# Kernel optimization log

Hardware: AMD Instinct MI355X
Metric: run time of the kernel (lower is better)

Reference implementation:

```python
import jax, jax.numpy as jnp
import numpy as np

S, I, H = 4096, 2048, 2048


def setup_inputs() -> dict:
    key = jax.random.key(0)
    ks = jax.random.split(key, 7)
    k = 1.0 / np.sqrt(H)  # torch LSTMCell init range (values don't affect math shape)
    x = jax.random.normal(ks[0], (S, I), dtype=jnp.float32)
    W_ih = jax.random.uniform(ks[1], (4 * H, I), minval=-k, maxval=k, dtype=jnp.float32)
    W_hh = jax.random.uniform(ks[2], (4 * H, H), minval=-k, maxval=k, dtype=jnp.float32)
    b_ih = jax.random.uniform(ks[3], (4 * H,), minval=-k, maxval=k, dtype=jnp.float32)
    b_hh = jax.random.uniform(ks[4], (4 * H,), minval=-k, maxval=k, dtype=jnp.float32)
    xav = np.sqrt(2.0 / (1 + H))  # xavier_normal_ std for a (1, H) tensor
    h0 = jax.random.normal(ks[5], (1, H), dtype=jnp.float32) * xav
    c0 = jax.random.normal(ks[6], (1, H), dtype=jnp.float32) * xav
    return {"x": x, "W_ih": W_ih, "W_hh": W_hh, "b_ih": b_ih, "b_hh": b_hh, "h0": h0, "c0": c0}


def reference(x, W_ih, W_hh, b_ih, b_hh, h0, c0):
    # Precompute input contribution for all timesteps in one big GEMM: (S, 4H)
    x_gates = x @ W_ih.T + b_ih + b_hh
    W_hh_T = W_hh.T  # (H, 4H)

    def step(carry, xg_t):
        h, c = carry  # each (H,)
        gates = xg_t + h @ W_hh_T  # (4H,)
        i, f, g, o = jnp.split(gates, 4)
        i = jax.nn.sigmoid(i)
        f = jax.nn.sigmoid(f)
        g = jnp.tanh(g)
        o = jax.nn.sigmoid(o)
        c_new = f * c + i * g
        h_new = o * jnp.tanh(c_new)
        return (h_new, c_new), h_new

    _, hs = jax.lax.scan(step, (h0[0], c0[0]), x_gates)
    return hs[:, None, :]  # (S, 1, H) matching torch.stack of (1, H) states
```

## Files before the change

kernel.cpp:

```cpp
#include <hip/hip_runtime.h>
#include <hip/hip_bf16.h>

#define S_LEN 4096
#define IDIM  2048
#define HDIM  2048
#define G4    8192
#define NB    256
#define TPB   512
#define SENT  0x7FC00000u

typedef __attribute__((ext_vector_type(2))) float  f32x2;
typedef __attribute__((ext_vector_type(4))) float  f32x4;
typedef __attribute__((ext_vector_type(8))) short  bf16x8;

#define PKFMA(acc, w, h) \
  asm("v_pk_fma_f32 %0, %1, %2, %0" : "+v"(acc) : "v"(w), "v"(h))

__device__ __forceinline__ unsigned short f2bf(float f) {
  unsigned u = __float_as_uint(f);
  unsigned r = (u + 0x7FFFu + ((u >> 16) & 1u)) >> 16;
  return (unsigned short)r;
}
__device__ __forceinline__ float bf2f(unsigned short h) {
  return __uint_as_float(((unsigned)h) << 16);
}
__device__ __forceinline__ float sigmoid_fast(float x) {
  return __builtin_amdgcn_rcpf(1.f + __expf(-x));
}
__device__ __forceinline__ float tanh_fast(float x) {
  return 1.f - 2.f * __builtin_amdgcn_rcpf(__expf(2.f * x) + 1.f);
}

__global__ __launch_bounds__(256) void fill_sentinel(unsigned long long* p) {
  const unsigned long long v =
      ((unsigned long long)SENT << 32) | (unsigned long long)SENT;
  const int n = S_LEN * HDIM / 2;
  for (int i = blockIdx.x * 256 + threadIdx.x; i < n; i += gridDim.x * 256)
    p[i] = v;
}

#define BM 128
#define BKK 32
#define LDK 40

__global__ __launch_bounds__(256) void gemm_xg_mfma(
    const float* __restrict__ x, const float* __restrict__ Wih,
    const float* __restrict__ bih, const float* __restrict__ bhh,
    unsigned short* __restrict__ xg) {
  __shared__ unsigned short As[BM][LDK];
  __shared__ unsigned short Bs[BM][LDK];

  const int t = threadIdx.x;
  const int lane = t & 63, wid = t >> 6;
  const int wr = wid >> 1, wc = wid & 1;

  int bid = ((int)blockIdx.x & 7) * 256 + ((int)blockIdx.x >> 3);
  const int s0 = (bid >> 6) * BM;
  const int j0 = (bid & 63) * BM;

  f32x4 acc[4][4] = {};

  float bias[4];
#pragma unroll
  for (int n = 0; n < 4; ++n) {
    const int col = j0 + wc * 64 + n * 16 + (lane & 15);
    bias[n] = bih[col] + bhh[col];
  }

  for (int k0 = 0; k0 < IDIM; k0 += BKK) {
    float4 va[4], vb[4];
#pragma unroll
    for (int u = 0; u < 4; ++u) {
      const int f = t + 256 * u;
      const int row = f >> 3, kc = (f & 7) * 4;
      va[u] = *(const float4*)&x  [(size_t)(s0 + row) * IDIM + k0 + kc];
      vb[u] = *(const float4*)&Wih[(size_t)(j0 + row) * IDIM + k0 + kc];
    }
    __syncthreads();
#pragma unroll
    for (int u = 0; u < 4; ++u) {
      const int f = t + 256 * u;
      const int row = f >> 3, kc = (f & 7) * 4;
      ushort4 pa, pb;
      pa.x = f2bf(va[u].x); pa.y = f2bf(va[u].y);
      pa.z = f2bf(va[u].z); pa.w = f2bf(va[u].w);
      pb.x = f2bf(vb[u].x); pb.y = f2bf(vb[u].y);
      pb.z = f2bf(vb[u].z); pb.w = f2bf(vb[u].w);
      *(ushort4*)&As[row][kc] = pa;
      *(ushort4*)&Bs[row][kc] = pb;
    }
    __syncthreads();

    const int fr = lane & 15, koff = (lane >> 4) * 8;
    bf16x8 a[4], bfr[4];
#pragma unroll
    for (int m = 0; m < 4; ++m)
      a[m] = *(const bf16x8*)&As[wr * 64 + m * 16 + fr][koff];
#pragma unroll
    for (int n = 0; n < 4; ++n)
      bfr[n] = *(const bf16x8*)&Bs[wc * 64 + n * 16 + fr][koff];
#pragma unroll
    for (int m = 0; m < 4; ++m)
#pragma unroll
      for (int n = 0; n < 4; ++n)
        acc[m][n] = __builtin_amdgcn_mfma_f32_16x16x32_bf16(
            a[m], bfr[n], acc[m][n], 0, 0, 0);
  }

#pragma unroll
  for (int m = 0; m < 4; ++m) {
    const int row0 = s0 + wr * 64 + m * 16 + (lane >> 4) * 4;
#pragma unroll
    for (int n = 0; n < 4; ++n) {
      const int col = j0 + wc * 64 + n * 16 + (lane & 15);
#pragma unroll
      for (int r = 0; r < 4; ++r)
        xg[(size_t)(row0 + r) * G4 + col] = f2bf(acc[m][n][r] + bias[n]);
    }
  }
}

__global__ __launch_bounds__(TPB, 2) void lstm_scan(
    const unsigned short* __restrict__ xg, const float* __restrict__ Whh,
    const float* __restrict__ h0, const float* __restrict__ c0,
    float* __restrict__ out, unsigned* __restrict__ flags) {
  __shared__ __align__(16) float h_sh[HDIM];

  const int b = blockIdx.x, t = threadIdx.x;
  const int lane = t & 63, wid = t >> 6;
  const int j = b * 8 + wid;

  f32x2 w2[4][16];
#pragma unroll
  for (int g = 0; g < 4; ++g) {
    const float* wp = Whh + ((size_t)g * HDIM + j) * HDIM + lane * 4;
#pragma unroll
    for (int i = 0; i < 8; ++i) {
      const float4 v = *(const float4*)(wp + i * 256);
      w2[g][i * 2 + 0] = f32x2{v.x, v.y};
      w2[g][i * 2 + 1] = f32x2{v.z, v.w};
    }
  }
  float c_reg = (lane == 0) ? c0[j] : 0.f;

  for (int ts = 0; ts < S_LEN; ++ts) {
    float xgv = 0.f;
    if (lane < 4)
      xgv = bf2f(xg[(size_t)ts * G4 + (size_t)lane * HDIM + j]);

    if (ts == 0) {
      __syncthreads();
      h_sh[2*t]        = h0[2*t];
      h_sh[2*t + 1]    = h0[2*t + 1];
      h_sh[2*t + 1024] = h0[2*t + 1024];
      h_sh[2*t + 1025] = h0[2*t + 1025];
    } else {
      if (wid == 0) {
        const unsigned want = (unsigned)ts;
        unsigned f0 = 0, f1 = 0, f2 = 0, f3 = 0;
        for (;;) {
          if (f0 < want) f0 = __hip_atomic_load(&flags[lane],       __ATOMIC_RELAXED, __HIP_MEMORY_SCOPE_AGENT);
          if (f1 < want) f1 = __hip_atomic_load(&flags[lane +  64], __ATOMIC_RELAXED, __HIP_MEMORY_SCOPE_AGENT);
          if (f2 < want) f2 = __hip_atomic_load(&flags[lane + 128], __ATOMIC_RELAXED, __HIP_MEMORY_SCOPE_AGENT);
          if (f3 < want) f3 = __hip_atomic_load(&flags[lane + 192], __ATOMIC_RELAXED, __HIP_MEMORY_SCOPE_AGENT);
          if (f0 >= want && f1 >= want && f2 >= want && f3 >= want) break;
          __builtin_amdgcn_s_sleep(1);
        }
      }
      __syncthreads();
      const unsigned long long* src =
          (const unsigned long long*)(out + (size_t)(ts - 1) * HDIM);
      unsigned long long r0, r1;
      do {
        r0 = __hip_atomic_load(src + t, __ATOMIC_RELAXED,
                               __HIP_MEMORY_SCOPE_AGENT);
      } while (((unsigned)r0 == SENT) | ((unsigned)(r0 >> 32) == SENT));
      do {
        r1 = __hip_atomic_load(src + t + 512, __ATOMIC_RELAXED,
                               __HIP_MEMORY_SCOPE_AGENT);
      } while (((unsigned)r1 == SENT) | ((unsigned)(r1 >> 32) == SENT));
      h_sh[2*t]        = __uint_as_float((unsigned)r0);
      h_sh[2*t + 1]    = __uint_as_float((unsigned)(r0 >> 32));
      h_sh[2*t + 1024] = __uint_as_float((unsigned)r1);
      h_sh[2*t + 1025] = __uint_as_float((unsigned)(r1 >> 32));
    }
    __syncthreads();

    f32x2 A0 = {0.f, 0.f}, A1 = {0.f, 0.f}, A2 = {0.f, 0.f}, A3 = {0.f, 0.f};
    const f32x4* h4 = (const f32x4*)&h_sh[lane * 4];
#pragma unroll
    for (int i = 0; i < 8; ++i) {
      const f32x4 hv = h4[i * 64];
      const f32x2 hlo = {hv.x, hv.y}, hhi = {hv.z, hv.w};
      PKFMA(A0, w2[0][i*2+0], hlo); PKFMA(A0, w2[0][i*2+1], hhi);
      PKFMA(A1, w2[1][i*2+0], hlo); PKFMA(A1, w2[1][i*2+1], hhi);
      PKFMA(A2, w2[2][i*2+0], hlo); PKFMA(A2, w2[2][i*2+1], hhi);
      PKFMA(A3, w2[3][i*2+0], hlo); PKFMA(A3, w2[3][i*2+1], hhi);
    }
    float a0 = A0.x + A0.y, a1 = A1.x + A1.y;
    float a2 = A2.x + A2.y, a3 = A3.x + A3.y;
#pragma unroll
    for (int m = 1; m < 64; m <<= 1) {
      a0 += __shfl_xor(a0, m);
      a1 += __shfl_xor(a1, m);
      a2 += __shfl_xor(a2, m);
      a3 += __shfl_xor(a3, m);
    }
    float sv = (lane == 0) ? a0 : (lane == 1) ? a1 : (lane == 2) ? a2 : a3;
    sv += xgv;
    const float av = (lane == 2) ? tanh_fast(sv) : sigmoid_fast(sv);
    const float iv = __shfl(av, 0);
    const float fv = __shfl(av, 1);
    const float gv = __shfl(av, 2);
    const float ov = __shfl(av, 3);
    if (lane == 0) {
      c_reg = fmaf(fv, c_reg, iv * gv);
      const float hn = ov * tanh_fast(c_reg);
      __hip_atomic_store(&out[(size_t)ts * HDIM + j], hn,
                         __ATOMIC_RELAXED, __HIP_MEMORY_SCOPE_AGENT);
    }
    asm volatile("" ::: "memory");
    __builtin_amdgcn_s_barrier();
    asm volatile("" ::: "memory");
    if (t == 0)
      __hip_atomic_store(&flags[b], (unsigned)(ts + 1),
                         __ATOMIC_RELAXED, __HIP_MEMORY_SCOPE_AGENT);
  }
}

extern "C" void kernel_launch(void* const* d_in, const int* in_sizes, int n_in,
                              void* d_out, int out_size, void* d_ws, size_t ws_size,
                              hipStream_t stream) {
  const float* x   = (const float*)d_in[0];
  const float* Wih = (const float*)d_in[1];
  const float* Whh = (const float*)d_in[2];
  const float* bih = (const float*)d_in[3];
  const float* bhh = (const float*)d_in[4];
  const float* h0  = (const float*)d_in[5];
  const float* c0  = (const float*)d_in[6];
  float* out = (float*)d_out;

  unsigned* flags = (unsigned*)d_ws;
  unsigned short* xg = (unsigned short*)((char*)d_ws + 32768);

  hipMemsetAsync(flags, 0, NB * sizeof(unsigned), stream);

  fill_sentinel<<<dim3(2048), 256, 0, stream>>>((unsigned long long*)out);
  gemm_xg_mfma<<<dim3(2048), 256, 0, stream>>>(x, Wih, bih, bhh, xg);

  void* args[] = {(void*)&xg, (void*)&Whh, (void*)&h0,
                  (void*)&c0, (void*)&out, (void*)&flags};
  hipLaunchCooperativeKernel((void*)lstm_scan, dim3(NB), dim3(TPB),
                             args, 0, stream);
}
```

Before: 12.23 ms.

## Store recurrent weights as packed bf16 in registers and restage h layout

```diff
diff --git a/kernel.cpp b/kernel.cpp
--- a/kernel.cpp
+++ b/kernel.cpp
@@ -23,6 +23,15 @@
 }
 __device__ __forceinline__ float bf2f(unsigned short h) {
   return __uint_as_float(((unsigned)h) << 16);
+}
+__device__ __forceinline__ f32x2 bfpair(unsigned u) {
+  f32x2 r;
+  r.x = __uint_as_float(u << 16);
+  r.y = __uint_as_float(u & 0xFFFF0000u);
+  return r;
+}
+__device__ __forceinline__ f32x2 mk2(float a, float b) {
+  f32x2 r; r.x = a; r.y = b; return r;
 }
 __device__ __forceinline__ float sigmoid_fast(float x) {
   return __builtin_amdgcn_rcpf(1.f + __expf(-x));
@@ -120,83 +129,86 @@
   }
 }
 
+
+__device__ __forceinline__ void stage_pair(float* hA, float* hB, int k,
+                                           float v0, float v1) {
+  const int c = k >> 9, r = (k >> 3) & 63, e = k & 7;
+  float* dst = ((e & 4) ? hB : hA) + c * 256 + r * 4 + (e & 3);
+  dst[0] = v0;
+  dst[1] = v1;
+}
+
+#define DGC(Acc, g, c, HA, HB) do {                       \
+  const uint4 wv = w_reg[(g) * 4 + (c)];                  \
+  PKFMA(Acc, bfpair(wv.x), mk2(HA.x, HA.y));              \
+  PKFMA(Acc, bfpair(wv.y), mk2(HA.z, HA.w));              \
+  PKFMA(Acc, bfpair(wv.z), mk2(HB.x, HB.y));              \
+  PKFMA(Acc, bfpair(wv.w), mk2(HB.z, HB.w));              \
+} while (0)
+
 __global__ __launch_bounds__(TPB, 2) void lstm_scan(
     const unsigned short* __restrict__ xg, const float* __restrict__ Whh,
     const float* __restrict__ h0, const float* __restrict__ c0,
     float* __restrict__ out, unsigned* __restrict__ flags) {
-  __shared__ __align__(16) float h_sh[HDIM];
+  __shared__ __align__(16) float hA[1024];
+  __shared__ __align__(16) float hB[1024];
 
   const int b = blockIdx.x, t = threadIdx.x;
   const int lane = t & 63, wid = t >> 6;
   const int j = b * 8 + wid;
 
-  f32x2 w2[4][16];
+  uint4 w_reg[16];
 #pragma unroll
   for (int g = 0; g < 4; ++g) {
-    const float* wp = Whh + ((size_t)g * HDIM + j) * HDIM + lane * 4;
-#pragma unroll
-    for (int i = 0; i < 8; ++i) {
-      const float4 v = *(const float4*)(wp + i * 256);
-      w2[g][i * 2 + 0] = f32x2{v.x, v.y};
-      w2[g][i * 2 + 1] = f32x2{v.z, v.w};
-    }
-  }
+    const float* wp = Whh + ((size_t)g * HDIM + j) * HDIM;
+#pragma unroll
+    for (int c = 0; c < 4; ++c) {
+      const float4 q0 = *(const float4*)(wp + c * 512 + lane * 8);
+      const float4 q1 = *(const float4*)(wp + c * 512 + lane * 8 + 4);
+      uint4 pk;
+      pk.x = (unsigned)f2bf(q0.x) | ((unsigned)f2bf(q0.y) << 16);
+      pk.y = (unsigned)f2bf(q0.z) | ((unsigned)f2bf(q0.w) << 16);
+      pk.z = (unsigned)f2bf(q1.x) | ((unsigned)f2bf(q1.y) << 16);
+      pk.w = (unsigned)f2bf(q1.z) | ((unsigned)f2bf(q1.w) << 16);
+      asm volatile("" : "+v"(pk.x), "+v"(pk.y), "+v"(pk.z), "+v"(pk.w));
+      w_reg[g * 4 + c] = pk;
+    }
+  }
+
   float c_reg = (lane == 0) ? c0[j] : 0.f;
+
+  {
+    const float2 p0 = *(const float2*)&h0[2 * t];
+    const float2 p1 = *(const float2*)&h0[2 * t + 1024];
+    stage_pair(hA, hB, 2 * t, p0.x, p0.y);
+    stage_pair(hA, hB, 2 * t + 1024, p1.x, p1.y);
+  }
+  __syncthreads();
 
   for (int ts = 0; ts < S_LEN; ++ts) {
     float xgv = 0.f;
     if (lane < 4)
       xgv = bf2f(xg[(size_t)ts * G4 + (size_t)lane * HDIM + j]);
 
-    if (ts == 0) {
-      __syncthreads();
-      h_sh[2*t]        = h0[2*t];
-      h_sh[2*t + 1]    = h0[2*t + 1];
-      h_sh[2*t + 1024] = h0[2*t + 1024];
-      h_sh[2*t + 1025] = h0[2*t + 1025];
-    } else {
-      if (wid == 0) {
-        const unsigned want = (unsigned)ts;
-        unsigned f0 = 0, f1 = 0, f2 = 0, f3 = 0;
-        for (;;) {
-          if (f0 < want) f0 = __hip_atomic_load(&flags[lane],       __ATOMIC_RELAXED, __HIP_MEMORY_SCOPE_AGENT);
-          if (f1 < want) f1 = __hip_atomic_load(&flags[lane +  64], __ATOMIC_RELAXED, __HIP_MEMORY_SCOPE_AGENT);
-          if (f2 < want) f2 = __hip_atomic_load(&flags[lane + 128], __ATOMIC_RELAXED, __HIP_MEMORY_SCOPE_AGENT);
-          if (f3 < want) f3 = __hip_atomic_load(&flags[lane + 192], __ATOMIC_RELAXED, __HIP_MEMORY_SCOPE_AGENT);
-          if (f0 >= want && f1 >= want && f2 >= want && f3 >= want) break;
-          __builtin_amdgcn_s_sleep(1);
-        }
-      }
-      __syncthreads();
-      const unsigned long long* src =
-          (const unsigned long long*)(out + (size_t)(ts - 1) * HDIM);
-      unsigned long long r0, r1;
-      do {
-        r0 = __hip_atomic_load(src + t, __ATOMIC_RELAXED,
-                               __HIP_MEMORY_SCOPE_AGENT);
-      } while (((unsigned)r0 == SENT) | ((unsigned)(r0 >> 32) == SENT));
-      do {
-        r1 = __hip_atomic_load(src + t + 512, __ATOMIC_RELAXED,
-                               __HIP_MEMORY_SCOPE_AGENT);
-      } while (((unsigned)r1 == SENT) | ((unsigned)(r1 >> 32) == SENT));
-      h_sh[2*t]        = __uint_as_float((unsigned)r0);
-      h_sh[2*t + 1]    = __uint_as_float((unsigned)(r0 >> 32));
-      h_sh[2*t + 1024] = __uint_as_float((unsigned)r1);
-      h_sh[2*t + 1025] = __uint_as_float((unsigned)(r1 >> 32));
-    }
-    __syncthreads();
+    const f32x4 ha0 = *(const f32x4*)&hA[0 * 256 + lane * 4];
+    const f32x4 ha1 = *(const f32x4*)&hA[1 * 256 + lane * 4];
+    const f32x4 ha2 = *(const f32x4*)&hA[2 * 256 + lane * 4];
+    const f32x4 ha3 = *(const f32x4*)&hA[3 * 256 + lane * 4];
+    const f32x4 hb0 = *(const f32x4*)&hB[0 * 256 + lane * 4];
+    const f32x4 hb1 = *(const f32x4*)&hB[1 * 256 + lane * 4];
+    const f32x4 hb2 = *(const f32x4*)&hB[2 * 256 + lane * 4];
+    const f32x4 hb3 = *(const f32x4*)&hB[3 * 256 + lane * 4];
 
     f32x2 A0 = {0.f, 0.f}, A1 = {0.f, 0.f}, A2 = {0.f, 0.f}, A3 = {0.f, 0.f};
-    const f32x4* h4 = (const f32x4*)&h_sh[lane * 4];
-#pragma unroll
-    for (int i = 0; i < 8; ++i) {
-      const f32x4 hv = h4[i * 64];
-      const f32x2 hlo = {hv.x, hv.y}, hhi = {hv.z, hv.w};
-      PKFMA(A0, w2[0][i*2+0], hlo); PKFMA(A0, w2[0][i*2+1], hhi);
-      PKFMA(A1, w2[1][i*2+0], hlo); PKFMA(A1, w2[1][i*2+1], hhi);
-      PKFMA(A2, w2[2][i*2+0], hlo); PKFMA(A2, w2[2][i*2+1], hhi);
-      PKFMA(A3, w2[3][i*2+0], hlo); PKFMA(A3, w2[3][i*2+1], hhi);
-    }
+    DGC(A0, 0, 0, ha0, hb0); DGC(A0, 0, 1, ha1, hb1);
+    DGC(A0, 0, 2, ha2, hb2); DGC(A0, 0, 3, ha3, hb3);
+    DGC(A1, 1, 0, ha0, hb0); DGC(A1, 1, 1, ha1, hb1);
+    DGC(A1, 1, 2, ha2, hb2); DGC(A1, 1, 3, ha3, hb3);
+    DGC(A2, 2, 0, ha0, hb0); DGC(A2, 2, 1, ha1, hb1);
+    DGC(A2, 2, 2, ha2, hb2); DGC(A2, 2, 3, ha3, hb3);
+    DGC(A3, 3, 0, ha0, hb0); DGC(A3, 3, 1, ha1, hb1);
+    DGC(A3, 3, 2, ha2, hb2); DGC(A3, 3, 3, ha3, hb3);
+
     float a0 = A0.x + A0.y, a1 = A1.x + A1.y;
     float a2 = A2.x + A2.y, a3 = A3.x + A3.y;
 #pragma unroll
@@ -219,12 +231,42 @@
       __hip_atomic_store(&out[(size_t)ts * HDIM + j], hn,
                          __ATOMIC_RELAXED, __HIP_MEMORY_SCOPE_AGENT);
     }
-    asm volatile("" ::: "memory");
     __builtin_amdgcn_s_barrier();
-    asm volatile("" ::: "memory");
     if (t == 0)
       __hip_atomic_store(&flags[b], (unsigned)(ts + 1),
                          __ATOMIC_RELAXED, __HIP_MEMORY_SCOPE_AGENT);
+
+    if (ts + 1 == S_LEN) break;
+
+    if (wid == 0) {
+      const unsigned want = (unsigned)(ts + 1);
+      unsigned f0 = 0, f1 = 0, f2 = 0, f3 = 0;
+      for (;;) {
+        if (f0 < want) f0 = __hip_atomic_load(&flags[lane],       __ATOMIC_RELAXED, __HIP_MEMORY_SCOPE_AGENT);
+        if (f1 < want) f1 = __hip_atomic_load(&flags[lane +  64], __ATOMIC_RELAXED, __HIP_MEMORY_SCOPE_AGENT);
+        if (f2 < want) f2 = __hip_atomic_load(&flags[lane + 128], __ATOMIC_RELAXED, __HIP_MEMORY_SCOPE_AGENT);
+        if (f3 < want) f3 = __hip_atomic_load(&flags[lane + 192], __ATOMIC_RELAXED, __HIP_MEMORY_SCOPE_AGENT);
+        if (f0 >= want && f1 >= want && f2 >= want && f3 >= want) break;
+        __builtin_amdgcn_s_sleep(1);
+      }
+    }
+    __syncthreads();
+    const unsigned long long* src =
+        (const unsigned long long*)(out + (size_t)ts * HDIM);
+    unsigned long long r0, r1;
+    do {
+      r0 = __hip_atomic_load(src + t, __ATOMIC_RELAXED,
+                             __HIP_MEMORY_SCOPE_AGENT);
+    } while (((unsigned)r0 == SENT) | ((unsigned)(r0 >> 32) == SENT));
+    do {
+      r1 = __hip_atomic_load(src + t + 512, __ATOMIC_RELAXED,
+                             __HIP_MEMORY_SCOPE_AGENT);
+    } while (((unsigned)r1 == SENT) | ((unsigned)(r1 >> 32) == SENT));
+    stage_pair(hA, hB, 2 * t,
+               __uint_as_float((unsigned)r0), __uint_as_float((unsigned)(r0 >> 32)));
+    stage_pair(hA, hB, 2 * t + 1024,
+               __uint_as_float((unsigned)r1), __uint_as_float((unsigned)(r1 >> 32)));
+    __syncthreads();
   }
 }
 
```

New measurement: 18.89 ms. +54.5%, slower.

## Stage bf16 W_hh in LDS and prefetch weights during the inter-block wait

Applied to the files above, without the earlier changes.

```diff
diff --git a/kernel.cpp b/kernel.cpp
--- a/kernel.cpp
+++ b/kernel.cpp
@@ -23,6 +23,15 @@
 }
 __device__ __forceinline__ float bf2f(unsigned short h) {
   return __uint_as_float(((unsigned)h) << 16);
+}
+__device__ __forceinline__ f32x2 bfpair(unsigned u) {
+  f32x2 r;
+  r.x = __uint_as_float(u << 16);
+  r.y = __uint_as_float(u & 0xFFFF0000u);
+  return r;
+}
+__device__ __forceinline__ f32x2 mk2(float a, float b) {
+  f32x2 r; r.x = a; r.y = b; return r;
 }
 __device__ __forceinline__ float sigmoid_fast(float x) {
   return __builtin_amdgcn_rcpf(1.f + __expf(-x));
@@ -120,83 +129,92 @@
   }
 }
 
-__global__ __launch_bounds__(TPB, 2) void lstm_scan(
+
+#define LDW(g, i) \
+  (*(const uint4*)&Wlds[(wid * 4 + (g)) * 2048 + (i) * 512 + lane * 8])
+#define PIN4(v) \
+  asm volatile("" : "+v"(v.x), "+v"(v.y), "+v"(v.z), "+v"(v.w))
+#define WPREF do { \
+  w00 = LDW(0,0); w01 = LDW(0,1); w02 = LDW(0,2); w03 = LDW(0,3); \
+  w10 = LDW(1,0); w11 = LDW(1,1); w12 = LDW(1,2); w13 = LDW(1,3); \
+  w20 = LDW(2,0); w21 = LDW(2,1); w22 = LDW(2,2); w23 = LDW(2,3); \
+  w30 = LDW(3,0); w31 = LDW(3,1); w32 = LDW(3,2); w33 = LDW(3,3); \
+  PIN4(w00); PIN4(w01); PIN4(w02); PIN4(w03); \
+  PIN4(w10); PIN4(w11); PIN4(w12); PIN4(w13); \
+  PIN4(w20); PIN4(w21); PIN4(w22); PIN4(w23); \
+  PIN4(w30); PIN4(w31); PIN4(w32); PIN4(w33); \
+} while (0)
+
+#define DGC(Acc, W, HA, HB) do { \
+  PKFMA(Acc, bfpair(W.x), mk2(HA.x, HA.y)); \
+  PKFMA(Acc, bfpair(W.y), mk2(HA.z, HA.w)); \
+  PKFMA(Acc, bfpair(W.z), mk2(HB.x, HB.y)); \
+  PKFMA(Acc, bfpair(W.w), mk2(HB.z, HB.w)); \
+} while (0)
+
+__global__ __launch_bounds__(TPB, 1) void lstm_scan(
     const unsigned short* __restrict__ xg, const float* __restrict__ Whh,
     const float* __restrict__ h0, const float* __restrict__ c0,
     float* __restrict__ out, unsigned* __restrict__ flags) {
+  extern __shared__ unsigned short Wlds[];
   __shared__ __align__(16) float h_sh[HDIM];
 
   const int b = blockIdx.x, t = threadIdx.x;
   const int lane = t & 63, wid = t >> 6;
   const int j = b * 8 + wid;
 
-  f32x2 w2[4][16];
 #pragma unroll
   for (int g = 0; g < 4; ++g) {
-    const float* wp = Whh + ((size_t)g * HDIM + j) * HDIM + lane * 4;
-#pragma unroll
-    for (int i = 0; i < 8; ++i) {
-      const float4 v = *(const float4*)(wp + i * 256);
-      w2[g][i * 2 + 0] = f32x2{v.x, v.y};
-      w2[g][i * 2 + 1] = f32x2{v.z, v.w};
-    }
-  }
+    const float* wp = Whh + ((size_t)g * HDIM + j) * HDIM;
+#pragma unroll
+    for (int i = 0; i < 4; ++i) {
+      const float4 q0 = *(const float4*)(wp + i * 512 + lane * 8);
+      const float4 q1 = *(const float4*)(wp + i * 512 + lane * 8 + 4);
+      uint4 pk;
+      pk.x = (unsigned)f2bf(q0.x) | ((unsigned)f2bf(q0.y) << 16);
+      pk.y = (unsigned)f2bf(q0.z) | ((unsigned)f2bf(q0.w) << 16);
+      pk.z = (unsigned)f2bf(q1.x) | ((unsigned)f2bf(q1.y) << 16);
+      pk.w = (unsigned)f2bf(q1.z) | ((unsigned)f2bf(q1.w) << 16);
+      *(uint4*)&Wlds[(wid * 4 + g) * 2048 + i * 512 + lane * 8] = pk;
+    }
+  }
+
+  h_sh[t]        = h0[t];
+  h_sh[t + 512]  = h0[t + 512];
+  h_sh[t + 1024] = h0[t + 1024];
+  h_sh[t + 1536] = h0[t + 1536];
+  __syncthreads();
+
   float c_reg = (lane == 0) ? c0[j] : 0.f;
+
+  uint4 w00, w01, w02, w03, w10, w11, w12, w13,
+        w20, w21, w22, w23, w30, w31, w32, w33;
+  WPREF;
 
   for (int ts = 0; ts < S_LEN; ++ts) {
     float xgv = 0.f;
     if (lane < 4)
       xgv = bf2f(xg[(size_t)ts * G4 + (size_t)lane * HDIM + j]);
 
-    if (ts == 0) {
-      __syncthreads();
-      h_sh[2*t]        = h0[2*t];
-      h_sh[2*t + 1]    = h0[2*t + 1];
-      h_sh[2*t + 1024] = h0[2*t + 1024];
-      h_sh[2*t + 1025] = h0[2*t + 1025];
-    } else {
-      if (wid == 0) {
-        const unsigned want = (unsigned)ts;
-        unsigned f0 = 0, f1 = 0, f2 = 0, f3 = 0;
-        for (;;) {
-          if (f0 < want) f0 = __hip_atomic_load(&flags[lane],       __ATOMIC_RELAXED, __HIP_MEMORY_SCOPE_AGENT);
-          if (f1 < want) f1 = __hip_atomic_load(&flags[lane +  64], __ATOMIC_RELAXED, __HIP_MEMORY_SCOPE_AGENT);
-          if (f2 < want) f2 = __hip_atomic_load(&flags[lane + 128], __ATOMIC_RELAXED, __HIP_MEMORY_SCOPE_AGENT);
-          if (f3 < want) f3 = __hip_atomic_load(&flags[lane + 192], __ATOMIC_RELAXED, __HIP_MEMORY_SCOPE_AGENT);
-          if (f0 >= want && f1 >= want && f2 >= want && f3 >= want) break;
-          __builtin_amdgcn_s_sleep(1);
-        }
-      }
-      __syncthreads();
-      const unsigned long long* src =
-          (const unsigned long long*)(out + (size_t)(ts - 1) * HDIM);
-      unsigned long long r0, r1;
-      do {
-        r0 = __hip_atomic_load(src + t, __ATOMIC_RELAXED,
-                               __HIP_MEMORY_SCOPE_AGENT);
-      } while (((unsigned)r0 == SENT) | ((unsigned)(r0 >> 32) == SENT));
-      do {
-        r1 = __hip_atomic_load(src + t + 512, __ATOMIC_RELAXED,
-                               __HIP_MEMORY_SCOPE_AGENT);
-      } while (((unsigned)r1 == SENT) | ((unsigned)(r1 >> 32) == SENT));
-      h_sh[2*t]        = __uint_as_float((unsigned)r0);
-      h_sh[2*t + 1]    = __uint_as_float((unsigned)(r0 >> 32));
-      h_sh[2*t + 1024] = __uint_as_float((unsigned)r1);
-      h_sh[2*t + 1025] = __uint_as_float((unsigned)(r1 >> 32));
-    }
-    __syncthreads();
+    const f32x4 ha0 = *(const f32x4*)&h_sh[0 * 512 + lane * 8];
+    const f32x4 hb0 = *(const f32x4*)&h_sh[0 * 512 + lane * 8 + 4];
+    const f32x4 ha1 = *(const f32x4*)&h_sh[1 * 512 + lane * 8];
+    const f32x4 hb1 = *(const f32x4*)&h_sh[1 * 512 + lane * 8 + 4];
+    const f32x4 ha2 = *(const f32x4*)&h_sh[2 * 512 + lane * 8];
+    const f32x4 hb2 = *(const f32x4*)&h_sh[2 * 512 + lane * 8 + 4];
+    const f32x4 ha3 = *(const f32x4*)&h_sh[3 * 512 + lane * 8];
+    const f32x4 hb3 = *(const f32x4*)&h_sh[3 * 512 + lane * 8 + 4];
 
     f32x2 A0 = {0.f, 0.f}, A1 = {0.f, 0.f}, A2 = {0.f, 0.f}, A3 = {0.f, 0.f};
-    const f32x4* h4 = (const f32x4*)&h_sh[lane * 4];
-#pragma unroll
-    for (int i = 0; i < 8; ++i) {
-      const f32x4 hv = h4[i * 64];
-      const f32x2 hlo = {hv.x, hv.y}, hhi = {hv.z, hv.w};
-      PKFMA(A0, w2[0][i*2+0], hlo); PKFMA(A0, w2[0][i*2+1], hhi);
-      PKFMA(A1, w2[1][i*2+0], hlo); PKFMA(A1, w2[1][i*2+1], hhi);
-      PKFMA(A2, w2[2][i*2+0], hlo); PKFMA(A2, w2[2][i*2+1], hhi);
-      PKFMA(A3, w2[3][i*2+0], hlo); PKFMA(A3, w2[3][i*2+1], hhi);
-    }
+    DGC(A0, w00, ha0, hb0); DGC(A0, w01, ha1, hb1);
+    DGC(A0, w02, ha2, hb2); DGC(A0, w03, ha3, hb3);
+    DGC(A1, w10, ha0, hb0); DGC(A1, w11, ha1, hb1);
+    DGC(A1, w12, ha2, hb2); DGC(A1, w13, ha3, hb3);
+    DGC(A2, w20, ha0, hb0); DGC(A2, w21, ha1, hb1);
+    DGC(A2, w22, ha2, hb2); DGC(A2, w23, ha3, hb3);
+    DGC(A3, w30, ha0, hb0); DGC(A3, w31, ha1, hb1);
+    DGC(A3, w32, ha2, hb2); DGC(A3, w33, ha3, hb3);
+
     float a0 = A0.x + A0.y, a1 = A1.x + A1.y;
     float a2 = A2.x + A2.y, a3 = A3.x + A3.y;
 #pragma unroll
@@ -219,12 +237,44 @@
       __hip_atomic_store(&out[(size_t)ts * HDIM + j], hn,
                          __ATOMIC_RELAXED, __HIP_MEMORY_SCOPE_AGENT);
     }
-    asm volatile("" ::: "memory");
     __builtin_amdgcn_s_barrier();
-    asm volatile("" ::: "memory");
     if (t == 0)
       __hip_atomic_store(&flags[b], (unsigned)(ts + 1),
                          __ATOMIC_RELAXED, __HIP_MEMORY_SCOPE_AGENT);
+
+    if (ts + 1 == S_LEN) break;
+
+    WPREF;
+
+    if (wid == 0) {
+      const unsigned want = (unsigned)(ts + 1);
+      unsigned f0 = 0, f1 = 0, f2 = 0, f3 = 0;
+      for (;;) {
+        if (f0 < want) f0 = __hip_atomic_load(&flags[lane],       __ATOMIC_RELAXED, __HIP_MEMORY_SCOPE_AGENT);
+        if (f1 < want) f1 = __hip_atomic_load(&flags[lane +  64], __ATOMIC_RELAXED, __HIP_MEMORY_SCOPE_AGENT);
+        if (f2 < want) f2 = __hip_atomic_load(&flags[lane + 128], __ATOMIC_RELAXED, __HIP_MEMORY_SCOPE_AGENT);
+        if (f3 < want) f3 = __hip_atomic_load(&flags[lane + 192], __ATOMIC_RELAXED, __HIP_MEMORY_SCOPE_AGENT);
+        if (f0 >= want && f1 >= want && f2 >= want && f3 >= want) break;
+        __builtin_amdgcn_s_sleep(1);
+      }
+    }
+    __syncthreads();
+    const unsigned long long* src =
+        (const unsigned long long*)(out + (size_t)ts * HDIM);
+    unsigned long long r0, r1;
+    do {
+      r0 = __hip_atomic_load(src + t, __ATOMIC_RELAXED,
+                             __HIP_MEMORY_SCOPE_AGENT);
+    } while (((unsigned)r0 == SENT) | ((unsigned)(r0 >> 32) == SENT));
+    do {
+      r1 = __hip_atomic_load(src + t + 512, __ATOMIC_RELAXED,
+                             __HIP_MEMORY_SCOPE_AGENT);
+    } while (((unsigned)r1 == SENT) | ((unsigned)(r1 >> 32) == SENT));
+    h_sh[2*t]        = __uint_as_float((unsigned)r0);
+    h_sh[2*t + 1]    = __uint_as_float((unsigned)(r0 >> 32));
+    h_sh[2*t + 1024] = __uint_as_float((unsigned)r1);
+    h_sh[2*t + 1025] = __uint_as_float((unsigned)(r1 >> 32));
+    __syncthreads();
   }
 }
 
@@ -251,5 +301,5 @@
   void* args[] = {(void*)&xg, (void*)&Whh, (void*)&h0,
                   (void*)&c0, (void*)&out, (void*)&flags};
   hipLaunchCooperativeKernel((void*)lstm_scan, dim3(NB), dim3(TPB),
-                             args, 0, stream);
-}
+                             args, 131072 , stream);
+}
```

Result: slower. 16.06 ms (+31.3%).
